# Optimization experiments

Hardware: AMD Instinct MI355X
Metric: run time of the kernel (lower is better)

## Reference

```python
import jax, jax.numpy as jnp
import numpy as np

NUM_GRAPHS = 256
BN_EPS = 1e-5
GN_EPS = 1e-5


def setup_inputs() -> dict:
    key = jax.random.key(0)
    ks = jax.random.split(key, 8)
    N, E, D, H = 100000, 600000, 128, 128
    x = jax.random.normal(ks[0], (N, D), dtype=jnp.float32)
    W1 = jax.random.normal(ks[1], (4, 4 * H, D), dtype=jnp.float32) * 0.05
    bn_g = jnp.ones((4, 4 * H), dtype=jnp.float32)
    bn_b = jnp.zeros((4, 4 * H), dtype=jnp.float32)
    W2 = jax.random.normal(ks[2], (4, H, 4 * H), dtype=jnp.float32) * 0.05
    b2 = jnp.zeros((4, H), dtype=jnp.float32)
    gn_g = jnp.ones((4, H), dtype=jnp.float32)
    gn_b = jnp.zeros((4, H), dtype=jnp.float32)
    gn_a = jnp.ones((4, H), dtype=jnp.float32)
    edge_index = jax.random.randint(ks[3], (2, E), 0, N, dtype=jnp.int64)
    batch = jnp.sort(jax.random.randint(ks[4], (N,), 0, NUM_GRAPHS, dtype=jnp.int64))
    return {"x": x, "W1": W1, "bn_g": bn_g, "bn_b": bn_b, "W2": W2, "b2": b2,
            "gn_g": gn_g, "gn_b": gn_b, "gn_a": gn_a,
            "edge_index": edge_index, "batch": batch}


def reference(x, W1, bn_g, bn_b, W2, b2, gn_g, gn_b, gn_a, edge_index, batch):
    N = x.shape[0]
    src, dst = edge_index[0], edge_index[1]
    # per-graph node counts (shared by GraphNorm and mean-pool)
    cnt = jax.ops.segment_sum(jnp.ones((N,), x.dtype), batch, num_segments=NUM_GRAPHS)
    cnt = jnp.maximum(cnt, 1.0)[:, None]  # [G,1]

    h = x
    hs = []
    for l in range(4):  # fixed small layer loop
        # GINConv: (1+eps)*x + sum_{j->i} x_j, eps=0 default
        agg = jax.ops.segment_sum(h[src], dst, num_segments=N)
        z = h + agg
        # MLP: Linear(no bias) -> BatchNorm1d (batch stats) -> SELU -> Linear
        z = z @ W1[l].T
        mu = jnp.mean(z, axis=0)
        var = jnp.mean((z - mu) ** 2, axis=0)
        z = (z - mu) * jax.lax.rsqrt(var + BN_EPS) * bn_g[l] + bn_b[l]
        z = jax.nn.selu(z)
        z = z @ W2[l].T + b2[l]
        # GraphNorm: per-graph mean/var with learnable mean scale alpha
        gmean = jax.ops.segment_sum(z, batch, num_segments=NUM_GRAPHS) / cnt
        sub = z - gn_a[l] * gmean[batch]
        gvar = jax.ops.segment_sum(sub * sub, batch, num_segments=NUM_GRAPHS) / cnt
        z = gn_g[l] * sub * jax.lax.rsqrt(gvar[batch] + GN_EPS) + gn_b[l]
        z = jax.nn.selu(z)  # self.act (SELU, matching MLP)
        hs.append(z)
        h = z

    hg = jnp.concatenate(hs, axis=1)  # [N, 4*H]
    pooled = jax.ops.segment_sum(hg, batch, num_segments=NUM_GRAPHS) / cnt
    return pooled
```

## Files before the change

kernel.cpp:

```cpp
#include <hip/hip_runtime.h>
#include <hip/hip_bf16.h>


typedef __attribute__((ext_vector_type(8))) short bf16x8;
typedef __attribute__((ext_vector_type(4))) float f32x4;

__device__ __forceinline__ unsigned short f2b(float x){
    __hip_bfloat16 h = __float2bfloat16(x);
    return *reinterpret_cast<unsigned short*>(&h);
}
__device__ __forceinline__ float b2f(unsigned short u){
    __hip_bfloat16 h;
    *reinterpret_cast<unsigned short*>(&h) = u;
    return __bfloat162float(h);
}
__device__ __forceinline__ float selu_f(float x){
    const float sc = 1.0507009873554805f, al = 1.6732632423543772f;
    return x > 0.f ? sc * x : sc * al * (__expf(x) - 1.f);
}

__global__ void count_kernel(const int* __restrict__ dst, int* __restrict__ counts, int E){
    int e = blockIdx.x * 256 + threadIdx.x;
    if (e < E) atomicAdd(&counts[dst[e]], 1);
}

__global__ void cnt_bs_kernel(const int* __restrict__ batch, float* __restrict__ cnt, int N){
    __shared__ int sb[257];
    int g = threadIdx.x;
    int lo = 0, hi = N;
    while (lo < hi){ int mid = (lo + hi) >> 1; if (batch[mid] < g) lo = mid + 1; else hi = mid; }
    sb[g] = lo;
    if (g == 0) sb[256] = N;
    __syncthreads();
    cnt[g] = fmaxf((float)(sb[g + 1] - sb[g]), 1.f);
}

__global__ __launch_bounds__(1024) void scan_kernel(const int* __restrict__ counts,
                                                    int* __restrict__ row_ptr, int N){
    __shared__ int wsum[16];
    __shared__ int wpre[16];
    __shared__ int s_total;
    __shared__ int s_running;
    int tid = threadIdx.x;
    int lane = tid & 63, wid = tid >> 6;
    if (tid == 0) s_running = 0;
    __syncthreads();
    for (int base = 0; base < N; base += 4096){
        int idx0 = base + tid * 4;
        int v[4];
        #pragma unroll
        for (int j = 0; j < 4; j++) v[j] = (idx0 + j < N) ? counts[idx0 + j] : 0;
        int tsum = v[0] + v[1] + v[2] + v[3];
        int x = tsum;
        #pragma unroll
        for (int off = 1; off < 64; off <<= 1){
            int y = __shfl_up(x, off, 64);
            if (lane >= off) x += y;
        }
        if (lane == 63) wsum[wid] = x;
        __syncthreads();
        if (wid == 0 && lane < 16){
            int w = wsum[lane];
            int xx = w;
            #pragma unroll
            for (int off = 1; off < 16; off <<= 1){
                int y = __shfl_up(xx, off, 64);
                if (lane >= off) xx += y;
            }
            wpre[lane] = xx - w;
            if (lane == 15) s_total = xx;
        }
        __syncthreads();
        int run = s_running + wpre[wid] + (x - tsum);
        #pragma unroll
        for (int j = 0; j < 4; j++){
            if (idx0 + j < N) row_ptr[idx0 + j] = run;
            run += v[j];
        }
        __syncthreads();
        if (tid == 0) s_running += s_total;
        __syncthreads();
    }
    if (tid == 0) row_ptr[N] = s_running;
}

__global__ void fill_kernel(const int* __restrict__ ei, const int* __restrict__ row_ptr,
                            int* __restrict__ fill, int* __restrict__ colv, int E){
    int e = blockIdx.x * 256 + threadIdx.x;
    if (e < E){
        int s = ei[e];
        int d = ei[E + e];
        int pos = atomicAdd(&fill[d], 1);
        colv[row_ptr[d] + pos] = s;
    }
}

__global__ void pack_kernel(const float* __restrict__ W1, const float* __restrict__ W2,
                            unsigned short* __restrict__ W1p, unsigned short* __restrict__ W2p){
    int t = blockIdx.x * 256 + threadIdx.x;
    int which = t >> 15;
    int u = t & 32767;
    int lane = u & 63; u >>= 6;
    int nf = u & 3; u >>= 2;
    int wc = u & 1; u >>= 1;
    int kk = u & 3; u >>= 2;
    int c = u & 3; u >>= 2;
    int l = u;
    int col = wc * 64 + nf * 16 + (lane & 15);
    int kbase = kk * 32 + (lane >> 4) * 8;
    size_t ob = ((((((size_t)(l * 4 + c) * 4 + kk) * 2 + wc) * 4 + nf) * 2) * 512) + lane * 8;
    unsigned short* dst = which == 0 ? W1p : W2p;
    #pragma unroll
    for (int j = 0; j < 8; j++){
        int k = kbase + j;
        float wv = which == 0 ? W1[((size_t)(l * 512) + c * 128 + col) * 128 + k]
                              : W2[((size_t)(l * 128) + col) * 512 + c * 128 + k];
        unsigned short hi = f2b(wv);
        unsigned short lo = f2b(wv - b2f(hi));
        dst[ob + j] = hi;
        dst[ob + 512 + j] = lo;
    }
}

__global__ __launch_bounds__(256) void agg_split_kernel(
    const float* __restrict__ h, const int* __restrict__ row_ptr,
    const int* __restrict__ colv,
    unsigned short* __restrict__ zhi, unsigned short* __restrict__ zlo, int N)
{
    int t = blockIdx.x * 256 + threadIdx.x;
    int i = t >> 5;
    if (i >= N) return;
    int vo = (t & 31);
    const float4* hv = reinterpret_cast<const float4*>(h);
    int p0 = row_ptr[i], p1 = row_ptr[i + 1];
    float4 acc = hv[(size_t)i * 32 + vo];
    int p = p0;
    for (; p + 4 <= p1; p += 4){
        int s0 = colv[p], s1 = colv[p + 1], s2 = colv[p + 2], s3 = colv[p + 3];
        float4 a = hv[(size_t)s0 * 32 + vo];
        float4 b = hv[(size_t)s1 * 32 + vo];
        float4 c = hv[(size_t)s2 * 32 + vo];
        float4 d = hv[(size_t)s3 * 32 + vo];
        acc.x += (a.x + b.x) + (c.x + d.x);
        acc.y += (a.y + b.y) + (c.y + d.y);
        acc.z += (a.z + b.z) + (c.z + d.z);
        acc.w += (a.w + b.w) + (c.w + d.w);
    }
    for (; p < p1; p++){
        float4 a = hv[(size_t)colv[p] * 32 + vo];
        acc.x += a.x; acc.y += a.y; acc.z += a.z; acc.w += a.w;
    }
    float vals[4] = {acc.x, acc.y, acc.z, acc.w};
    unsigned int h01, h23, l01, l23;
    {
        unsigned short hh[4], ll[4];
        #pragma unroll
        for (int j = 0; j < 4; j++){
            hh[j] = f2b(vals[j]);
            ll[j] = f2b(vals[j] - b2f(hh[j]));
        }
        h01 = (unsigned int)hh[0] | ((unsigned int)hh[1] << 16);
        h23 = (unsigned int)hh[2] | ((unsigned int)hh[3] << 16);
        l01 = (unsigned int)ll[0] | ((unsigned int)ll[1] << 16);
        l23 = (unsigned int)ll[2] | ((unsigned int)ll[3] << 16);
    }
    uint2* ph = reinterpret_cast<uint2*>(zhi + (size_t)i * 128 + vo * 4);
    *ph = make_uint2(h01, h23);
    uint2* pl = reinterpret_cast<uint2*>(zlo + (size_t)i * 128 + vo * 4);
    *pl = make_uint2(l01, l23);
}

__global__ __launch_bounds__(512) void stats_k(
    const unsigned short* __restrict__ Ahi_g, const unsigned short* __restrict__ Alo_g,
    const unsigned short* __restrict__ Bp, float* __restrict__ bn_acc, int N)
{
    __shared__ __align__(16) unsigned short Ah[128][136];
    __shared__ __align__(16) unsigned short Al[128][136];
    int tid = threadIdx.x, lane = tid & 63, w = tid >> 6;
    int wr = w >> 2, wq = w & 3;
    int r_lo = lane & 15, kg = lane >> 4;
    int m0 = blockIdx.x * 128;

    {
        int r = tid >> 2, hf = tid & 3;
        int grow = m0 + r;
        #pragma unroll
        for (int j = 0; j < 4; j++){
            int kc = hf * 32 + j * 8;
            uint4 hvv = make_uint4(0, 0, 0, 0), lvv = make_uint4(0, 0, 0, 0);
            if (grow < N){
                hvv = *reinterpret_cast<const uint4*>(Ahi_g + (size_t)grow * 128 + kc);
                lvv = *reinterpret_cast<const uint4*>(Alo_g + (size_t)grow * 128 + kc);
            }
            *reinterpret_cast<uint4*>(&Ah[r][kc]) = hvv;
            *reinterpret_cast<uint4*>(&Al[r][kc]) = lvv;
        }
    }
    __syncthreads();

    int wc = wq >> 1;
    for (int c = 0; c < 4; c++){
        const bf16x8* Bv = reinterpret_cast<const bf16x8*>(Bp) + (size_t)c * 4096;
        f32x4 acc[4][2];
        #pragma unroll
        for (int i = 0; i < 4; i++)
            #pragma unroll
            for (int j = 0; j < 2; j++) acc[i][j] = (f32x4){0.f, 0.f, 0.f, 0.f};

        for (int kk = 0; kk < 4; kk++){
            bf16x8 bh[2], bl[2];
            #pragma unroll
            for (int nf = 0; nf < 2; nf++){
                int nfold = (wq & 1) * 2 + nf;
                int ob = ((kk * 2 + wc) * 4 + nfold) * 2;
                bh[nf] = Bv[(ob + 0) * 64 + lane];
                bl[nf] = Bv[(ob + 1) * 64 + lane];
            }
            bf16x8 ah[4], alr[4];
            #pragma unroll
            for (int mf = 0; mf < 4; mf++){
                int ar = wr * 64 + mf * 16 + r_lo;
                ah[mf]  = *reinterpret_cast<const bf16x8*>(&Ah[ar][kk * 32 + kg * 8]);
                alr[mf] = *reinterpret_cast<const bf16x8*>(&Al[ar][kk * 32 + kg * 8]);
            }
            #pragma unroll
            for (int mf = 0; mf < 4; mf++)
                #pragma unroll
                for (int nf = 0; nf < 2; nf++){
                    acc[mf][nf] = __builtin_amdgcn_mfma_f32_16x16x32_bf16(ah[mf],  bh[nf], acc[mf][nf], 0, 0, 0);
                    acc[mf][nf] = __builtin_amdgcn_mfma_f32_16x16x32_bf16(ah[mf],  bl[nf], acc[mf][nf], 0, 0, 0);
                    acc[mf][nf] = __builtin_amdgcn_mfma_f32_16x16x32_bf16(alr[mf], bh[nf], acc[mf][nf], 0, 0, 0);
                }
        }

        #pragma unroll
        for (int nf = 0; nf < 2; nf++){
            int col = wq * 32 + nf * 16 + r_lo;
            float s = 0.f, q = 0.f;
            #pragma unroll
            for (int mf = 0; mf < 4; mf++)
                #pragma unroll
                for (int r = 0; r < 4; r++){
                    int row = m0 + wr * 64 + mf * 16 + kg * 4 + r;
                    if (row < N){
                        float v = acc[mf][nf][r];
                        s += v; q += v * v;
                    }
                }
            s += __shfl_xor(s, 16); s += __shfl_xor(s, 32);
            q += __shfl_xor(q, 16); q += __shfl_xor(q, 32);
            if (lane < 16){
                atomicAdd(&bn_acc[c * 256 + col], s);
                atomicAdd(&bn_acc[c * 256 + 128 + col], q);
            }
        }
    }
}

__global__ void bn_final_k(const float* __restrict__ bn_acc,
                           const float* __restrict__ bng, const float* __restrict__ bnb,
                           float* __restrict__ sc, float* __restrict__ sh,
                           int l, float invN){
    int colg = threadIdx.x;
    float s = bn_acc[(colg >> 7) * 256 + (colg & 127)];
    float q = bn_acc[(colg >> 7) * 256 + 128 + (colg & 127)];
    float mu = s * invN;
    float var = q * invN - mu * mu;
    float inv = rsqrtf(var + 1e-5f);
    float g = bng[l * 512 + colg] * inv;
    sc[colg] = g;
    sh[colg] = bnb[l * 512 + colg] - mu * g;
}

__global__ __launch_bounds__(512, 1) void fused_k(
    const unsigned short* __restrict__ Ahi_g, const unsigned short* __restrict__ Alo_g,
    const unsigned short* __restrict__ B1p, const unsigned short* __restrict__ B2p,
    float* __restrict__ Z, const float* __restrict__ bsc, const float* __restrict__ bsh,
    const float* __restrict__ b2l, int N)
{
    __shared__ __align__(16) unsigned short Ah[128][136];
    __shared__ __align__(16) unsigned short Al[128][136];
    __shared__ __align__(16) unsigned short Ph[128][136];
    __shared__ __align__(16) unsigned short Pl[128][136];
    __shared__ float s_sc[512], s_sh[512];
    int tid = threadIdx.x, lane = tid & 63, w = tid >> 6;
    int wr = w >> 2, wq = w & 3;
    int r_lo = lane & 15, kg = lane >> 4;
    int m0 = blockIdx.x * 128;

    if (tid < 512){ s_sc[tid] = bsc[tid]; s_sh[tid] = bsh[tid]; }
    {
        int r = tid >> 2, hf = tid & 3;
        int grow = m0 + r;
        #pragma unroll
        for (int j = 0; j < 4; j++){
            int kc = hf * 32 + j * 8;
            uint4 hvv = make_uint4(0, 0, 0, 0), lvv = make_uint4(0, 0, 0, 0);
            if (grow < N){
                hvv = *reinterpret_cast<const uint4*>(Ahi_g + (size_t)grow * 128 + kc);
                lvv = *reinterpret_cast<const uint4*>(Alo_g + (size_t)grow * 128 + kc);
            }
            *reinterpret_cast<uint4*>(&Ah[r][kc]) = hvv;
            *reinterpret_cast<uint4*>(&Al[r][kc]) = lvv;
        }
    }
    __syncthreads();

    int wc = wq >> 1;
    f32x4 acc2[4][2];
    #pragma unroll
    for (int i = 0; i < 4; i++)
        #pragma unroll
        for (int j = 0; j < 2; j++) acc2[i][j] = (f32x4){0.f, 0.f, 0.f, 0.f};

    for (int c = 0; c < 4; c++){
        f32x4 acc1[4][2];
        #pragma unroll
        for (int i = 0; i < 4; i++)
            #pragma unroll
            for (int j = 0; j < 2; j++) acc1[i][j] = (f32x4){0.f, 0.f, 0.f, 0.f};

        const bf16x8* B1v = reinterpret_cast<const bf16x8*>(B1p) + (size_t)c * 4096;
        for (int kk = 0; kk < 4; kk++){
            bf16x8 bh[2], bl[2];
            #pragma unroll
            for (int nf = 0; nf < 2; nf++){
                int nfold = (wq & 1) * 2 + nf;
                int ob = ((kk * 2 + wc) * 4 + nfold) * 2;
                bh[nf] = B1v[(ob + 0) * 64 + lane];
                bl[nf] = B1v[(ob + 1) * 64 + lane];
            }
            bf16x8 ah[4], alr[4];
            #pragma unroll
            for (int mf = 0; mf < 4; mf++){
                int ar = wr * 64 + mf * 16 + r_lo;
                ah[mf]  = *reinterpret_cast<const bf16x8*>(&Ah[ar][kk * 32 + kg * 8]);
                alr[mf] = *reinterpret_cast<const bf16x8*>(&Al[ar][kk * 32 + kg * 8]);
            }
            #pragma unroll
            for (int mf = 0; mf < 4; mf++)
                #pragma unroll
                for (int nf = 0; nf < 2; nf++){
                    acc1[mf][nf] = __builtin_amdgcn_mfma_f32_16x16x32_bf16(ah[mf],  bh[nf], acc1[mf][nf], 0, 0, 0);
                    acc1[mf][nf] = __builtin_amdgcn_mfma_f32_16x16x32_bf16(ah[mf],  bl[nf], acc1[mf][nf], 0, 0, 0);
                    acc1[mf][nf] = __builtin_amdgcn_mfma_f32_16x16x32_bf16(alr[mf], bh[nf], acc1[mf][nf], 0, 0, 0);
                }
        }

        __syncthreads();
        #pragma unroll
        for (int nf = 0; nf < 2; nf++){
            int colk = wq * 32 + nf * 16 + r_lo;
            float scv = s_sc[c * 128 + colk], shv = s_sh[c * 128 + colk];
            #pragma unroll
            for (int mf = 0; mf < 4; mf++)
                #pragma unroll
                for (int r = 0; r < 4; r++){
                    int rl = wr * 64 + mf * 16 + kg * 4 + r;
                    float t = selu_f(fmaf(acc1[mf][nf][r], scv, shv));
                    unsigned short hi = f2b(t);
                    Ph[rl][colk] = hi;
                    Pl[rl][colk] = f2b(t - b2f(hi));
                }
        }
        __syncthreads();

        const bf16x8* B2v = reinterpret_cast<const bf16x8*>(B2p);
        for (int kk2 = 0; kk2 < 4; kk2++){
            int kkf = c * 4 + kk2;
            bf16x8 bh[2], bl[2];
            #pragma unroll
            for (int nf = 0; nf < 2; nf++){
                int nfold = (wq & 1) * 2 + nf;
                int ob = ((kkf * 2 + wc) * 4 + nfold) * 2;
                bh[nf] = B2v[(ob + 0) * 64 + lane];
                bl[nf] = B2v[(ob + 1) * 64 + lane];
            }
            bf16x8 ah[4], alr[4];
            #pragma unroll
            for (int mf = 0; mf < 4; mf++){
                int ar = wr * 64 + mf * 16 + r_lo;
                ah[mf]  = *reinterpret_cast<const bf16x8*>(&Ph[ar][kk2 * 32 + kg * 8]);
                alr[mf] = *reinterpret_cast<const bf16x8*>(&Pl[ar][kk2 * 32 + kg * 8]);
            }
            #pragma unroll
            for (int mf = 0; mf < 4; mf++)
                #pragma unroll
                for (int nf = 0; nf < 2; nf++){
                    acc2[mf][nf] = __builtin_amdgcn_mfma_f32_16x16x32_bf16(ah[mf],  bh[nf], acc2[mf][nf], 0, 0, 0);
                    acc2[mf][nf] = __builtin_amdgcn_mfma_f32_16x16x32_bf16(ah[mf],  bl[nf], acc2[mf][nf], 0, 0, 0);
                    acc2[mf][nf] = __builtin_amdgcn_mfma_f32_16x16x32_bf16(alr[mf], bh[nf], acc2[mf][nf], 0, 0, 0);
                }
        }
    }

    #pragma unroll
    for (int nf = 0; nf < 2; nf++){
        int col = wq * 32 + nf * 16 + r_lo;
        float bv = b2l[col];
        #pragma unroll
        for (int mf = 0; mf < 4; mf++)
            #pragma unroll
            for (int r = 0; r < 4; r++){
                int row = m0 + wr * 64 + mf * 16 + kg * 4 + r;
                if (row < N)
                    Z[(size_t)row * 128 + col] = bv + acc2[mf][nf][r];
            }
    }
}

__global__ __launch_bounds__(256) void gn_stats_kernel(
    const float* __restrict__ z2, const int* __restrict__ batch,
    float* __restrict__ gsum, float* __restrict__ gsq, int N)
{
    __shared__ int sb[128];
    int tid = threadIdx.x;
    int base = blockIdx.x * 128;
    int end = min(128, N - base);
    if (tid < 128) sb[tid] = (tid < end) ? batch[base + tid] : 0;
    __syncthreads();
    int vo = tid & 31;
    int r0 = (tid >> 5) * 16;
    if (r0 >= end) return;
    int rend = min(r0 + 16, end);
    const float4* zv = reinterpret_cast<const float4*>(z2);
    float sx = 0.f, sy = 0.f, sz = 0.f, sw = 0.f;
    float qx = 0.f, qy = 0.f, qz = 0.f, qw = 0.f;
    int run_g = sb[r0];
    for (int r = r0; r < rend; r++){
        int g = sb[r];
        if (g != run_g){
            float* gs = &gsum[run_g * 128 + vo * 4];
            float* gq = &gsq[run_g * 128 + vo * 4];
            atomicAdd(gs + 0, sx); atomicAdd(gs + 1, sy); atomicAdd(gs + 2, sz); atomicAdd(gs + 3, sw);
            atomicAdd(gq + 0, qx); atomicAdd(gq + 1, qy); atomicAdd(gq + 2, qz); atomicAdd(gq + 3, qw);
            sx = sy = sz = sw = 0.f; qx = qy = qz = qw = 0.f;
            run_g = g;
        }
        float4 v = zv[(size_t)(base + r) * 32 + vo];
        sx += v.x; sy += v.y; sz += v.z; sw += v.w;
        qx += v.x * v.x; qy += v.y * v.y; qz += v.z * v.z; qw += v.w * v.w;
    }
    float* gs = &gsum[run_g * 128 + vo * 4];
    float* gq = &gsq[run_g * 128 + vo * 4];
    atomicAdd(gs + 0, sx); atomicAdd(gs + 1, sy); atomicAdd(gs + 2, sz); atomicAdd(gs + 3, sw);
    atomicAdd(gq + 0, qx); atomicAdd(gq + 1, qy); atomicAdd(gq + 2, qz); atomicAdd(gq + 3, qw);
}

__global__ void gn_final_kernel(float* __restrict__ gsum, float* __restrict__ gsq,
                                const float* __restrict__ cnt,
                                const float* __restrict__ gng, const float* __restrict__ gnb,
                                const float* __restrict__ gna,
                                float* __restrict__ scale, float* __restrict__ shift, int l){
    int g = blockIdx.x, c = threadIdx.x;
    int idx = g * 128 + c;
    float n = cnt[g];
    float m = gsum[idx] / n;
    float e2 = gsq[idx] / n;
    float a = gna[l * 128 + c];
    float var = e2 - (2.f * a - a * a) * m * m;
    float inv = rsqrtf(var + 1e-5f);
    float sc = gng[l * 128 + c] * inv;
    scale[idx] = sc;
    shift[idx] = gnb[l * 128 + c] - a * m * sc;
    gsum[idx] = 0.f;
    gsq[idx] = 0.f;
}

__global__ __launch_bounds__(256) void gn_apply_kernel(
    float* __restrict__ z2h, const int* __restrict__ batch,
    const float* __restrict__ scale, const float* __restrict__ shift,
    float* __restrict__ pool, int l, int N)
{
    __shared__ int sb[128];
    int tid = threadIdx.x;
    int base = blockIdx.x * 128;
    int end = min(128, N - base);
    if (tid < 128) sb[tid] = (tid < end) ? batch[base + tid] : 0;
    __syncthreads();
    int vo = tid & 31;
    int r0 = (tid >> 5) * 16;
    if (r0 >= end) return;
    int rend = min(r0 + 16, end);
    float4* zv = reinterpret_cast<float4*>(z2h);
    int run_g = sb[r0];
    float scx = scale[run_g * 128 + vo * 4 + 0], shx = shift[run_g * 128 + vo * 4 + 0];
    float scy = scale[run_g * 128 + vo * 4 + 1], shy = shift[run_g * 128 + vo * 4 + 1];
    float scz = scale[run_g * 128 + vo * 4 + 2], shz = shift[run_g * 128 + vo * 4 + 2];
    float scw = scale[run_g * 128 + vo * 4 + 3], shw = shift[run_g * 128 + vo * 4 + 3];
    float px = 0.f, py = 0.f, pz = 0.f, pw = 0.f;
    for (int r = r0; r < rend; r++){
        int g = sb[r];
        if (g != run_g){
            float* pp = &pool[run_g * 512 + l * 128 + vo * 4];
            atomicAdd(pp + 0, px); atomicAdd(pp + 1, py); atomicAdd(pp + 2, pz); atomicAdd(pp + 3, pw);
            px = py = pz = pw = 0.f;
            run_g = g;
            scx = scale[g * 128 + vo * 4 + 0]; shx = shift[g * 128 + vo * 4 + 0];
            scy = scale[g * 128 + vo * 4 + 1]; shy = shift[g * 128 + vo * 4 + 1];
            scz = scale[g * 128 + vo * 4 + 2]; shz = shift[g * 128 + vo * 4 + 2];
            scw = scale[g * 128 + vo * 4 + 3]; shw = shift[g * 128 + vo * 4 + 3];
        }
        size_t idx = (size_t)(base + r) * 32 + vo;
        float4 v = zv[idx];
        v.x = selu_f(fmaf(v.x, scx, shx));
        v.y = selu_f(fmaf(v.y, scy, shy));
        v.z = selu_f(fmaf(v.z, scz, shz));
        v.w = selu_f(fmaf(v.w, scw, shw));
        zv[idx] = v;
        px += v.x; py += v.y; pz += v.z; pw += v.w;
    }
    float* pp = &pool[run_g * 512 + l * 128 + vo * 4];
    atomicAdd(pp + 0, px); atomicAdd(pp + 1, py); atomicAdd(pp + 2, pz); atomicAdd(pp + 3, pw);
}

__global__ void final_kernel(const float* __restrict__ pool, const float* __restrict__ cnt,
                             float* __restrict__ out, int n){
    int i = blockIdx.x * 256 + threadIdx.x;
    if (i < n) out[i] = pool[i] / cnt[i >> 9];
}

extern "C" void kernel_launch(void* const* d_in, const int* in_sizes, int n_in,
                              void* d_out, int out_size, void* d_ws, size_t ws_size,
                              hipStream_t stream){
    const float* x    = (const float*)d_in[0];
    const float* W1   = (const float*)d_in[1];
    const float* bng  = (const float*)d_in[2];
    const float* bnb  = (const float*)d_in[3];
    const float* W2   = (const float*)d_in[4];
    const float* b2   = (const float*)d_in[5];
    const float* gng  = (const float*)d_in[6];
    const float* gnb  = (const float*)d_in[7];
    const float* gna  = (const float*)d_in[8];
    const int*   ei   = (const int*)d_in[9];
    const int*   batch= (const int*)d_in[10];
    int N = in_sizes[0] / 128;
    int E = in_sizes[9] / 2;
    float* out = (float*)d_out;
    int RB = (N + 127) / 128;

    char* ws = (char*)d_ws;
    size_t off = 0;
    auto alloc = [&](size_t bytes) -> char* {
        char* p = ws + off;
        off += (bytes + 255) & ~(size_t)255;
        return p;
    };
    unsigned short* z0hi = (unsigned short*)alloc((size_t)N * 128 * 2);
    unsigned short* z0lo = (unsigned short*)alloc((size_t)N * 128 * 2);
    float* z2     = (float*)alloc((size_t)N * 128 * 4);
    unsigned short* W1p = (unsigned short*)alloc(524288 * 2);
    unsigned short* W2p = (unsigned short*)alloc(524288 * 2);
    int*   row_ptr= (int*)alloc((size_t)(N + 1) * 4);
    int*   colv   = (int*)alloc((size_t)E * 4);
    int*   counts = (int*)alloc((size_t)N * 4);
    int*   fill   = (int*)alloc((size_t)N * 4);
    float* cnt_f  = (float*)alloc(256 * 4);
    float* bn_acc = (float*)alloc(16 * 256 * 4);
    float* bn_sc  = (float*)alloc(512 * 4);
    float* bn_sh  = (float*)alloc(512 * 4);
    float* gn_sum = (float*)alloc(256 * 128 * 4);
    float* gn_sq  = (float*)alloc(256 * 128 * 4);
    float* gn_sc  = (float*)alloc(256 * 128 * 4);
    float* gn_sh  = (float*)alloc(256 * 128 * 4);
    float* pool   = (float*)alloc(256 * 512 * 4);
    (void)ws_size;

    hipMemsetAsync(counts, 0, (size_t)N * 4, stream);
    hipMemsetAsync(fill,   0, (size_t)N * 4, stream);
    hipMemsetAsync(bn_acc, 0, 16 * 256 * 4, stream);
    hipMemsetAsync(gn_sum, 0, 2 * 256 * 128 * 4, stream);
    hipMemsetAsync(pool,   0, 256 * 512 * 4, stream);

    pack_kernel<<<256, 256, 0, stream>>>(W1, W2, W1p, W2p);
    count_kernel<<<(E + 255) / 256, 256, 0, stream>>>(ei + E, counts, E);
    scan_kernel<<<1, 1024, 0, stream>>>(counts, row_ptr, N);
    fill_kernel<<<(E + 255) / 256, 256, 0, stream>>>(ei, row_ptr, fill, colv, E);
    cnt_bs_kernel<<<1, 256, 0, stream>>>(batch, cnt_f, N);

    const float* hcur = x;
    float invN = 1.f / (float)N;
    for (int l = 0; l < 4; l++){
        agg_split_kernel<<<(N + 7) / 8, 256, 0, stream>>>(hcur, row_ptr, colv, z0hi, z0lo, N);
        stats_k<<<RB, 512, 0, stream>>>(z0hi, z0lo, W1p + (size_t)l * 131072,
                                        bn_acc + l * 1024, N);
        bn_final_k<<<1, 512, 0, stream>>>(bn_acc + l * 1024, bng, bnb,
                                          bn_sc, bn_sh, l, invN);
        fused_k<<<RB, 512, 0, stream>>>(z0hi, z0lo, W1p + (size_t)l * 131072,
                                        W2p + (size_t)l * 131072, z2,
                                        bn_sc, bn_sh, b2 + l * 128, N);
        gn_stats_kernel<<<RB, 256, 0, stream>>>(z2, batch, gn_sum, gn_sq, N);
        gn_final_kernel<<<256, 128, 0, stream>>>(gn_sum, gn_sq, cnt_f, gng, gnb, gna,
                                                 gn_sc, gn_sh, l);
        gn_apply_kernel<<<RB, 256, 0, stream>>>(z2, batch, gn_sc, gn_sh, pool, l, N);
        hcur = z2;
    }
    final_kernel<<<(out_size + 255) / 256, 256, 0, stream>>>(pool, cnt_f, out, out_size);
}
```

Before: 1.445 ms.

## Transpose first GEMM in fused MLP to stream Z from global and pack P stores

The first GEMM of the fused MLP kernel now treats the weights as the A operand and the node features as the B operand. Z hi/lo fragments are loaded directly from global memory into registers instead of being staged through shared memory, which removes the Ah/Al LDS buffers and the initial barrier. Because of the transposed accumulator layout, the SELU epilogue can pack four bf16 values and write them to Ph/Pl as 64-bit stores instead of scalar 16-bit stores. The lower LDS footprint allows launch bounds of 4 blocks per CU, but Z is now re-read from global memory once per c-chunk, four times in total, relying on the cache.

```diff
diff --git a/kernel.cpp b/kernel.cpp
--- a/kernel.cpp
+++ b/kernel.cpp
@@ -272,14 +272,12 @@
     sh[colg] = bnb[l * 512 + colg] - mu * g;
 }
 
-__global__ __launch_bounds__(512, 1) void fused_k(
-    const unsigned short* __restrict__ Ahi_g, const unsigned short* __restrict__ Alo_g,
+__global__ __launch_bounds__(512, 4) void fused_k(
+    const unsigned short* __restrict__ Zhi_g, const unsigned short* __restrict__ Zlo_g,
     const unsigned short* __restrict__ B1p, const unsigned short* __restrict__ B2p,
     float* __restrict__ Z, const float* __restrict__ bsc, const float* __restrict__ bsh,
     const float* __restrict__ b2l, int N)
 {
-    __shared__ __align__(16) unsigned short Ah[128][136];
-    __shared__ __align__(16) unsigned short Al[128][136];
     __shared__ __align__(16) unsigned short Ph[128][136];
     __shared__ __align__(16) unsigned short Pl[128][136];
     __shared__ float s_sc[512], s_sh[512];
@@ -289,22 +287,6 @@
     int m0 = blockIdx.x * 128;
 
     if (tid < 512){ s_sc[tid] = bsc[tid]; s_sh[tid] = bsh[tid]; }
-    {
-        int r = tid >> 2, hf = tid & 3;
-        int grow = m0 + r;
-        #pragma unroll
-        for (int j = 0; j < 4; j++){
-            int kc = hf * 32 + j * 8;
-            uint4 hvv = make_uint4(0, 0, 0, 0), lvv = make_uint4(0, 0, 0, 0);
-            if (grow < N){
-                hvv = *reinterpret_cast<const uint4*>(Ahi_g + (size_t)grow * 128 + kc);
-                lvv = *reinterpret_cast<const uint4*>(Alo_g + (size_t)grow * 128 + kc);
-            }
-            *reinterpret_cast<uint4*>(&Ah[r][kc]) = hvv;
-            *reinterpret_cast<uint4*>(&Al[r][kc]) = lvv;
-        }
-    }
-    __syncthreads();
 
     int wc = wq >> 1;
     f32x4 acc2[4][2];
@@ -313,55 +295,71 @@
         #pragma unroll
         for (int j = 0; j < 2; j++) acc2[i][j] = (f32x4){0.f, 0.f, 0.f, 0.f};
 
+    const bf16x8 zero8 = {0, 0, 0, 0, 0, 0, 0, 0};
+
     for (int c = 0; c < 4; c++){
-        f32x4 acc1[4][2];
-        #pragma unroll
-        for (int i = 0; i < 4; i++)
-            #pragma unroll
-            for (int j = 0; j < 2; j++) acc1[i][j] = (f32x4){0.f, 0.f, 0.f, 0.f};
+        f32x4 acc1[2][4];
+        #pragma unroll
+        for (int i = 0; i < 2; i++)
+            #pragma unroll
+            for (int j = 0; j < 4; j++) acc1[i][j] = (f32x4){0.f, 0.f, 0.f, 0.f};
 
         const bf16x8* B1v = reinterpret_cast<const bf16x8*>(B1p) + (size_t)c * 4096;
         for (int kk = 0; kk < 4; kk++){
-            bf16x8 bh[2], bl[2];
-            #pragma unroll
-            for (int nf = 0; nf < 2; nf++){
-                int nfold = (wq & 1) * 2 + nf;
-                int ob = ((kk * 2 + wc) * 4 + nfold) * 2;
-                bh[nf] = B1v[(ob + 0) * 64 + lane];
-                bl[nf] = B1v[(ob + 1) * 64 + lane];
-            }
-            bf16x8 ah[4], alr[4];
-            #pragma unroll
-            for (int mf = 0; mf < 4; mf++){
-                int ar = wr * 64 + mf * 16 + r_lo;
-                ah[mf]  = *reinterpret_cast<const bf16x8*>(&Ah[ar][kk * 32 + kg * 8]);
-                alr[mf] = *reinterpret_cast<const bf16x8*>(&Al[ar][kk * 32 + kg * 8]);
-            }
-            #pragma unroll
-            for (int mf = 0; mf < 4; mf++)
+            bf16x8 awh[2], awl[2];
+            #pragma unroll
+            for (int mfp = 0; mfp < 2; mfp++){
+                int colblk = wq * 2 + mfp;
+                int wc1 = colblk >> 2, nf1 = colblk & 3;
+                int ob = ((kk * 2 + wc1) * 4 + nf1) * 2;
+                awh[mfp] = B1v[(ob + 0) * 64 + lane];
+                awl[mfp] = B1v[(ob + 1) * 64 + lane];
+            }
+            bf16x8 bzh[4], bzl[4];
+            #pragma unroll
+            for (int nfp = 0; nfp < 4; nfp++){
+                int row = m0 + wr * 64 + nfp * 16 + r_lo;
+                if (row < N){
+                    size_t go = (size_t)row * 128 + kk * 32 + kg * 8;
+                    bzh[nfp] = *reinterpret_cast<const bf16x8*>(Zhi_g + go);
+                    bzl[nfp] = *reinterpret_cast<const bf16x8*>(Zlo_g + go);
+                } else { bzh[nfp] = zero8; bzl[nfp] = zero8; }
+            }
+            #pragma unroll
+            for (int mfp = 0; mfp < 2; mfp++)
                 #pragma unroll
-                for (int nf = 0; nf < 2; nf++){
-                    acc1[mf][nf] = __builtin_amdgcn_mfma_f32_16x16x32_bf16(ah[mf],  bh[nf], acc1[mf][nf], 0, 0, 0);
-                    acc1[mf][nf] = __builtin_amdgcn_mfma_f32_16x16x32_bf16(ah[mf],  bl[nf], acc1[mf][nf], 0, 0, 0);
-                    acc1[mf][nf] = __builtin_amdgcn_mfma_f32_16x16x32_bf16(alr[mf], bh[nf], acc1[mf][nf], 0, 0, 0);
+                for (int nfp = 0; nfp < 4; nfp++){
+                    acc1[mfp][nfp] = __builtin_amdgcn_mfma_f32_16x16x32_bf16(awh[mfp], bzh[nfp], acc1[mfp][nfp], 0, 0, 0);
+                    acc1[mfp][nfp] = __builtin_amdgcn_mfma_f32_16x16x32_bf16(awh[mfp], bzl[nfp], acc1[mfp][nfp], 0, 0, 0);
+                    acc1[mfp][nfp] = __builtin_amdgcn_mfma_f32_16x16x32_bf16(awl[mfp], bzh[nfp], acc1[mfp][nfp], 0, 0, 0);
                 }
         }
 
         __syncthreads();
         #pragma unroll
-        for (int nf = 0; nf < 2; nf++){
-            int colk = wq * 32 + nf * 16 + r_lo;
-            float scv = s_sc[c * 128 + colk], shv = s_sh[c * 128 + colk];
-            #pragma unroll
-            for (int mf = 0; mf < 4; mf++)
-                #pragma unroll
-                for (int r = 0; r < 4; r++){
-                    int rl = wr * 64 + mf * 16 + kg * 4 + r;
-                    float t = selu_f(fmaf(acc1[mf][nf][r], scv, shv));
-                    unsigned short hi = f2b(t);
-                    Ph[rl][colk] = hi;
-                    Pl[rl][colk] = f2b(t - b2f(hi));
-                }
+        for (int mfp = 0; mfp < 2; mfp++){
+            int ckb = wq * 32 + mfp * 16 + kg * 4;
+            float sc0 = s_sc[c * 128 + ckb + 0], sh0 = s_sh[c * 128 + ckb + 0];
+            float sc1 = s_sc[c * 128 + ckb + 1], sh1 = s_sh[c * 128 + ckb + 1];
+            float sc2 = s_sc[c * 128 + ckb + 2], sh2 = s_sh[c * 128 + ckb + 2];
+            float sc3 = s_sc[c * 128 + ckb + 3], sh3 = s_sh[c * 128 + ckb + 3];
+            #pragma unroll
+            for (int nfp = 0; nfp < 4; nfp++){
+                float t0 = selu_f(fmaf(acc1[mfp][nfp][0], sc0, sh0));
+                float t1 = selu_f(fmaf(acc1[mfp][nfp][1], sc1, sh1));
+                float t2 = selu_f(fmaf(acc1[mfp][nfp][2], sc2, sh2));
+                float t3 = selu_f(fmaf(acc1[mfp][nfp][3], sc3, sh3));
+                unsigned short h0 = f2b(t0), h1 = f2b(t1), h2 = f2b(t2), h3 = f2b(t3);
+                unsigned short l0 = f2b(t0 - b2f(h0)), l1 = f2b(t1 - b2f(h1));
+                unsigned short l2 = f2b(t2 - b2f(h2)), l3 = f2b(t3 - b2f(h3));
+                int node = wr * 64 + nfp * 16 + r_lo;
+                uint2 hv = make_uint2((unsigned int)h0 | ((unsigned int)h1 << 16),
+                                      (unsigned int)h2 | ((unsigned int)h3 << 16));
+                uint2 lv = make_uint2((unsigned int)l0 | ((unsigned int)l1 << 16),
+                                      (unsigned int)l2 | ((unsigned int)l3 << 16));
+                *reinterpret_cast<uint2*>(&Ph[node][ckb]) = hv;
+                *reinterpret_cast<uint2*>(&Pl[node][ckb]) = lv;
+            }
         }
         __syncthreads();
 
```

New measurement: 2.038 ms. 41.0% more time.
